# Kernel tuning notes

Measured on AMD Instinct MI355X. Metric: run time of the kernel, lower is better.

Reference implementation:

```python
import jax, jax.numpy as jnp
from jax import lax
import numpy as np

B, N, DIM = 2, 2048, 1024
HEADS, DIM_HEAD = 16, 64
KERNELS = (0, 3, 5, 7)
GROUPS = len(KERNELS)
HPG = HEADS // GROUPS          # heads per group = 4
CG = HPG * DIM_HEAD            # channels per group for depthwise conv = 256
INNER = HEADS * DIM_HEAD       # 1024


def _alibi_slopes(n):
    # power-of-2 branch of LearnedAlibiPosBias._get_slopes (n=4 here)
    start = 2.0 ** (-(2.0 ** -(np.log2(n) - 3)))
    return np.array([start * start ** i for i in range(n)], dtype=np.float32)


def setup_inputs() -> dict:
    key = jax.random.key(0)
    ks = jax.random.split(key, 24)
    d = {}
    d['x'] = jax.random.normal(ks[0], (B, N, DIM), jnp.float32)
    d['ln_gamma'] = jnp.ones((DIM,), jnp.float32)
    d['ln_beta'] = jnp.zeros((DIM,), jnp.float32)
    d['w_qkv'] = jax.random.normal(ks[1], (3 * INNER, DIM), jnp.float32) * 0.02
    i = 2
    for p in ('q', 'k', 'v'):
        for ksz in (3, 5, 7):
            d[f'dw{p}_w{ksz}'] = jax.random.normal(ks[i], (CG, 1, ksz), jnp.float32) * 0.1; i += 1
            d[f'dw{p}_b{ksz}'] = jax.random.normal(ks[i], (CG,), jnp.float32) * 0.02; i += 1
    # learned alibi slopes, initialized to the standard ALiBi values per group
    sl = _alibi_slopes(HPG).reshape(1, HPG, 1, 1)
    d['slopes'] = jnp.asarray(np.tile(sl, (GROUPS, 1, 1, 1)))
    d['w_out'] = jax.random.normal(ks[20], (DIM, INNER), jnp.float32) * 0.02
    return d


def _dw_causal_conv(xg, w, b, ksz):
    # xg: (B, CG, N); depthwise causal conv, left pad ksz-1
    xg = jnp.pad(xg, ((0, 0), (0, 0), (ksz - 1, 0)))
    out = lax.conv_general_dilated(xg, w, (1,), 'VALID',
                                   feature_group_count=CG,
                                   dimension_numbers=('NCH', 'OIH', 'NCH'))
    return out + b[None, :, None]


def _grouped_conv(t, w3, b3, w5, b5, w7, b7):
    # t: (B, INNER, N) channels laid out head-major; group g = channels [g*CG,(g+1)*CG)
    parts = [t[:, :CG]]  # group 0: kernel_size 0 -> Identity
    for i, (w, b, ksz) in enumerate(((w3, b3, 3), (w5, b5, 5), (w7, b7, 7))):
        parts.append(_dw_causal_conv(t[:, (i + 1) * CG:(i + 2) * CG], w, b, ksz))
    out = jnp.concatenate(parts, axis=1)                      # (B, INNER, N)
    out = out.reshape(B, HEADS, DIM_HEAD, N)
    return jnp.transpose(out, (0, 1, 3, 2))                   # (B, H, N, Dh)


def _forward(x, ln_gamma, ln_beta, w_qkv,
             dwq_w3, dwq_b3, dwq_w5, dwq_b5, dwq_w7, dwq_b7,
             dwk_w3, dwk_b3, dwk_w5, dwk_b5, dwk_w7, dwk_b7,
             dwv_w3, dwv_b3, dwv_w5, dwv_b5, dwv_w7, dwv_b7,
             slopes, w_out):
    scale = DIM_HEAD ** -0.5
    mu = jnp.mean(x, axis=-1, keepdims=True)
    var = jnp.var(x, axis=-1, keepdims=True)
    h = (x - mu) * lax.rsqrt(var + 1e-5) * ln_gamma + ln_beta   # (B, N, DIM)
    qkv = jnp.einsum('bnd,ed->ben', h, w_qkv)                   # (B, 3*INNER, N)
    q, k, v = jnp.split(qkv, 3, axis=1)
    q = _grouped_conv(q, dwq_w3, dwq_b3, dwq_w5, dwq_b5, dwq_w7, dwq_b7)
    k = _grouped_conv(k, dwk_w3, dwk_b3, dwk_w5, dwk_b5, dwk_w7, dwk_b7)
    v = _grouped_conv(v, dwv_w3, dwv_b3, dwv_w5, dwv_b5, dwv_w7, dwv_b7)
    sim = jnp.einsum('bhid,bhjd->bhij', q * scale, k)           # (B, H, N, N)
    idx = jnp.arange(N)
    dist = -jnp.abs(idx[None, :] - idx[:, None]).astype(sim.dtype)  # (N, N)
    bias = slopes.reshape(HEADS, 1, 1) * dist[None]             # (H, N, N)
    sim = sim + bias[None]
    causal = idx[None, :] > idx[:, None]                        # strictly future
    sim = jnp.where(causal[None, None], -jnp.finfo(sim.dtype).max, sim)
    attn = jax.nn.softmax(sim, axis=-1)
    out = jnp.einsum('bhij,bhjd->bhid', attn, v)                # (B, H, N, Dh)
    out = jnp.transpose(out, (0, 2, 1, 3)).reshape(B, N, INNER)
    return jnp.einsum('bne,de->bnd', out, w_out)


def reference(x, ln_gamma, ln_beta, w_qkv,
              dwq_w3, dwq_b3, dwq_w5, dwq_b5, dwq_w7, dwq_b7,
              dwk_w3, dwk_b3, dwk_w5, dwk_b5, dwk_w7, dwk_b7,
              dwv_w3, dwv_b3, dwv_w5, dwv_b5, dwv_w7, dwv_b7,
              slopes, w_out):
    return _forward(x, ln_gamma, ln_beta, w_qkv,
                    dwq_w3, dwq_b3, dwq_w5, dwq_b5, dwq_w7, dwq_b7,
                    dwk_w3, dwk_b3, dwk_w5, dwk_b5, dwk_w7, dwk_b7,
                    dwv_w3, dwv_b3, dwv_w5, dwv_b5, dwv_w7, dwv_b7,
                    slopes, w_out)
```

## Files before the change

### kernel.cpp

```cpp
#include <hip/hip_runtime.h>
#include <hip/hip_bf16.h>
#include <stdint.h>

typedef __bf16 bf8 __attribute__((ext_vector_type(8)));
typedef float  f4  __attribute__((ext_vector_type(4)));

constexpr int BATCH  = 2;
constexpr int SEQ    = 2048;
constexpr int DMODEL = 1024;
constexpr int NH     = 16;
constexpr int DHEAD  = 64;
constexpr int E3     = 3072;

static __device__ __forceinline__ f4 mfma16(bf8 a, bf8 b, f4 c){
  return __builtin_amdgcn_mfma_f32_16x16x32_bf16(a, b, c, 0, 0, 0);
}
static __device__ __forceinline__ uint32_t pack2(float a, float b){
  union { __bf16 h[2]; uint32_t u; } p;
  p.h[0] = (__bf16)a; p.h[1] = (__bf16)b;
  return p.u;
}
typedef const __attribute__((address_space(1))) uint32_t g_u32;
typedef __attribute__((address_space(3))) uint32_t l_u32;
static __device__ __forceinline__ void glds16(const __bf16* g, __bf16* l){
  __builtin_amdgcn_global_load_lds((g_u32*)g, (l_u32*)l, 16, 0, 0);
}

__global__ __launch_bounds__(256) void cvt_kernel(const float* __restrict__ s,
                                                  __bf16* __restrict__ d, int n){
  int i = (blockIdx.x * 256 + threadIdx.x) * 4;
  if(i < n){
    float4 v = *(const float4*)(s + i);
    __bf16 o[4] = {(__bf16)v.x, (__bf16)v.y, (__bf16)v.z, (__bf16)v.w};
    *(uint2*)(d + i) = *(const uint2*)o;
  }
}

__global__ __launch_bounds__(256) void ln_kernel(const float* __restrict__ x,
                                                 const float* __restrict__ gam,
                                                 const float* __restrict__ bet,
                                                 __bf16* __restrict__ h){
  int row = blockIdx.x;
  int tid = threadIdx.x;
  const float* xr = x + (size_t)row * DMODEL;
  float4 v = *(const float4*)(xr + tid*4);
  float s = v.x + v.y + v.z + v.w;
  float ss = v.x*v.x + v.y*v.y + v.z*v.z + v.w*v.w;
#pragma unroll
  for(int m=1;m<64;m<<=1){ s += __shfl_xor(s, m); ss += __shfl_xor(ss, m); }
  __shared__ float sm[8];
  int wid = tid >> 6;
  if((tid & 63) == 0){ sm[wid] = s; sm[4+wid] = ss; }
  __syncthreads();
  s  = sm[0]+sm[1]+sm[2]+sm[3];
  ss = sm[4]+sm[5]+sm[6]+sm[7];
  float mu  = s * (1.f/DMODEL);
  float var = ss * (1.f/DMODEL) - mu*mu;
  float r = rsqrtf(var + 1e-5f);
  float4 g = *(const float4*)(gam + tid*4);
  float4 bb = *(const float4*)(bet + tid*4);
  __bf16 o[4] = { (__bf16)((v.x-mu)*r*g.x + bb.x), (__bf16)((v.y-mu)*r*g.y + bb.y),
                  (__bf16)((v.z-mu)*r*g.z + bb.z), (__bf16)((v.w-mu)*r*g.w + bb.w) };
  *(uint2*)(h + (size_t)row*DMODEL + tid*4) = *(uint2*)o;
}

template<typename CT>
__global__ __launch_bounds__(256) void gemm_nt(const __bf16* __restrict__ A,
                                               const __bf16* __restrict__ Bm,
                                               CT* __restrict__ C,
                                               int M, int Ncols, int K){
  __shared__ __align__(16) __bf16 As[128*32];
  __shared__ __align__(16) __bf16 Bs[128*32];
  int m0 = blockIdx.y * 128, n0 = blockIdx.x * 128;
  int tid = threadIdx.x;
  int lane = tid & 63, wid = tid >> 6;
  int quad = lane >> 4, l15 = lane & 15;
  int wm = (wid >> 1) * 64, wn = (wid & 1) * 64;
  f4 acc[4][4] = {};
  int r0 = wid*32 + (lane >> 2);
  int cofs = (lane & 3) * 8;
  const __bf16* ag = A  + (size_t)(m0 + r0) * K + cofs;
  const __bf16* bg = Bm + (size_t)(n0 + r0) * K + cofs;
  __bf16* asb0 = &As[(wid*32)*32];
  __bf16* asb1 = &As[(wid*32+16)*32];
  __bf16* bsb0 = &Bs[(wid*32)*32];
  __bf16* bsb1 = &Bs[(wid*32+16)*32];
  const size_t rowskip = (size_t)16 * K;
  for(int k0 = 0; k0 < K; k0 += 32){
    __syncthreads();
    glds16(ag + k0,           asb0);
    glds16(ag + rowskip + k0, asb1);
    glds16(bg + k0,           bsb0);
    glds16(bg + rowskip + k0, bsb1);
    __syncthreads();
    bf8 af[4], bfr[4];
#pragma unroll
    for(int i=0;i<4;i++){
      af[i]  = *(const bf8*)&As[(wm + i*16 + l15)*32 + quad*8];
      bfr[i] = *(const bf8*)&Bs[(wn + i*16 + l15)*32 + quad*8];
    }
#pragma unroll
    for(int mi=0;mi<4;mi++)
#pragma unroll
      for(int ni=0;ni<4;ni++)
        acc[mi][ni] = mfma16(af[mi], bfr[ni], acc[mi][ni]);
  }
#pragma unroll
  for(int mi=0;mi<4;mi++)
#pragma unroll
    for(int ni=0;ni<4;ni++)
#pragma unroll
      for(int r=0;r<4;r++){
        int row = m0 + wm + mi*16 + quad*4 + r;
        int col = n0 + wn + ni*16 + l15;
        C[(size_t)row*Ncols + col] = (CT)acc[mi][ni][r];
      }
}

template<typename CT>
__global__ __launch_bounds__(256) void gemm_nt64(const __bf16* __restrict__ A,
                                                 const __bf16* __restrict__ Bm,
                                                 CT* __restrict__ C,
                                                 int M, int Ncols, int K){
  __shared__ __align__(16) __bf16 As[128*32];
  __shared__ __align__(16) __bf16 Bs[64*32];
  int m0 = blockIdx.y * 128, n0 = blockIdx.x * 64;
  int tid = threadIdx.x;
  int lane = tid & 63, wid = tid >> 6;
  int quad = lane >> 4, l15 = lane & 15;
  int wm = wid * 32;
  f4 acc[2][4] = {};
  int ra = wid*32 + (lane >> 2);
  int rb = wid*16 + (lane >> 2);
  int cofs = (lane & 3) * 8;
  const __bf16* ag = A  + (size_t)(m0 + ra) * K + cofs;
  const __bf16* bg = Bm + (size_t)(n0 + rb) * K + cofs;
  __bf16* asb0 = &As[(wid*32)*32];
  __bf16* asb1 = &As[(wid*32+16)*32];
  __bf16* bsb  = &Bs[(wid*16)*32];
  const size_t rowskip = (size_t)16 * K;
  for(int k0 = 0; k0 < K; k0 += 32){
    __syncthreads();
    glds16(ag + k0,           asb0);
    glds16(ag + rowskip + k0, asb1);
    glds16(bg + k0,           bsb);
    __syncthreads();
    bf8 af[2], bfr[4];
#pragma unroll
    for(int i=0;i<2;i++)
      af[i]  = *(const bf8*)&As[(wm + i*16 + l15)*32 + quad*8];
#pragma unroll
    for(int i=0;i<4;i++)
      bfr[i] = *(const bf8*)&Bs[(i*16 + l15)*32 + quad*8];
#pragma unroll
    for(int mi=0;mi<2;mi++)
#pragma unroll
      for(int ni=0;ni<4;ni++)
        acc[mi][ni] = mfma16(af[mi], bfr[ni], acc[mi][ni]);
  }
#pragma unroll
  for(int mi=0;mi<2;mi++)
#pragma unroll
    for(int ni=0;ni<4;ni++)
#pragma unroll
      for(int r=0;r<4;r++){
        int row = m0 + wm + mi*16 + quad*4 + r;
        int col = n0 + ni*16 + l15;
        C[(size_t)row*Ncols + col] = (CT)acc[mi][ni][r];
      }
}

__global__ __launch_bounds__(256) void conv_kernel(const __bf16* __restrict__ qkv,
    __bf16* __restrict__ qo, __bf16* __restrict__ ko, __bf16* __restrict__ vt,
    const float* qw3,const float* qb3,const float* qw5,const float* qb5,const float* qw7,const float* qb7,
    const float* kw3,const float* kb3,const float* kw5,const float* kb5,const float* kw7,const float* kb7,
    const float* vw3,const float* vb3,const float* vw5,const float* vb5,const float* vw7,const float* vb7){
  __shared__ __align__(16) __bf16 tile[72*256];
  int nc = blockIdx.x;
  int ec = blockIdx.y;
  int b  = blockIdx.z;
  int tid = threadIdx.x;
  int n0 = nc * 64;
  {
    int rrow = tid >> 5;
    int ccol = (tid & 31) * 8;
    const __bf16* src = qkv + (size_t)b*SEQ*E3 + ec*256 + ccol;
#pragma unroll
    for(int p=0;p<9;p++){
      int row = p*8 + rrow;
      int n = n0 - 8 + row;
      uint4 v = {0u,0u,0u,0u};
      if(n >= 0) v = *(const uint4*)(src + (size_t)n*E3);
      *(uint4*)&tile[row*256 + ccol] = v;
    }
  }
  __syncthreads();
  int e = ec*256 + tid;
  int p  = e >> 10;
  int c  = e & 1023;
  int g  = c >> 8;
  int cg = c & 255;
  int hh = c >> 6;
  int dh = c & 63;
  const float* W[9]  = {qw3,qw5,qw7,kw3,kw5,kw7,vw3,vw5,vw7};
  const float* Bp[9] = {qb3,qb5,qb7,kb3,kb5,kb7,vb3,vb5,vb7};
  int ksz = (g==0)?0:((g==1)?3:((g==2)?5:7));
  float w[7] = {0,0,0,0,0,0,0};
  float bias = 0.f;
  if(g > 0){
    const float* wp = W[p*3 + g - 1];
    const float* bp = Bp[p*3 + g - 1];
    for(int t=0;t<ksz;t++) w[t] = wp[cg*ksz + t];
    bias = bp[cg];
  }
  float xh[6];
#pragma unroll
  for(int i=0;i<6;i++) xh[i] = (float)tile[(2+i)*256 + tid];
  if(p == 2){
    __bf16* ob = vt + ((size_t)((b*NH + hh)*DHEAD + dh))*SEQ + n0;
    for(int blk=0; blk<8; blk++){
      __bf16 tmp[8];
#pragma unroll
      for(int u=0;u<8;u++){
        int dn = blk*8 + u;
        float cur = (float)tile[(8+dn)*256 + tid];
        float o;
        if(ksz == 0)      o = cur;
        else if(ksz == 3) o = w[0]*xh[4] + w[1]*xh[5] + w[2]*cur + bias;
        else if(ksz == 5) o = w[0]*xh[2] + w[1]*xh[3] + w[2]*xh[4] + w[3]*xh[5] + w[4]*cur + bias;
        else              o = w[0]*xh[0] + w[1]*xh[1] + w[2]*xh[2] + w[3]*xh[3] + w[4]*xh[4] + w[5]*xh[5] + w[6]*cur + bias;
        xh[0]=xh[1]; xh[1]=xh[2]; xh[2]=xh[3]; xh[3]=xh[4]; xh[4]=xh[5]; xh[5]=cur;
        tmp[u] = (__bf16)o;
      }
      *(uint4*)(ob + blk*8) = *(const uint4*)tmp;
    }
  } else {
    __bf16* outp = (p==0) ? qo : ko;
    __bf16* op = outp + ((size_t)(b*NH + hh)*SEQ)*DHEAD + dh;
#pragma unroll 4
    for(int dn=0; dn<64; dn++){
      float cur = (float)tile[(8+dn)*256 + tid];
      float o;
      if(ksz == 0)      o = cur;
      else if(ksz == 3) o = w[0]*xh[4] + w[1]*xh[5] + w[2]*cur + bias;
      else if(ksz == 5) o = w[0]*xh[2] + w[1]*xh[3] + w[2]*xh[4] + w[3]*xh[5] + w[4]*cur + bias;
      else              o = w[0]*xh[0] + w[1]*xh[1] + w[2]*xh[2] + w[3]*xh[3] + w[4]*xh[4] + w[5]*xh[5] + w[6]*cur + bias;
      xh[0]=xh[1]; xh[1]=xh[2]; xh[2]=xh[3]; xh[3]=xh[4]; xh[4]=xh[5]; xh[5]=cur;
      op[(size_t)(n0+dn)*DHEAD] = (__bf16)o;
    }
  }
}

__global__ __launch_bounds__(256) void attn_kernel(const __bf16* __restrict__ Qin,
                                                   const __bf16* __restrict__ Kin,
                                                   const __bf16* __restrict__ Vtin,
                                                   const float* __restrict__ slopes,
                                                   __bf16* __restrict__ Oout){
  __shared__ __align__(16) __bf16 Ks[2][64*72];
  __shared__ __align__(16) __bf16 Vts[2][64*72];
  __shared__ __align__(16) __bf16 Ps[4][16*72];
  __shared__ float Al[4][16];
  int bid = blockIdx.x;
  int pr = bid >> 5;
  int by = (bid & 7) + ((bid >> 3) & 3) * 8;
  int b  = by >> 4, hh = by & 15;
  int tid = threadIdx.x, lane = tid & 63, w = tid >> 6;
  int quad = lane >> 4, l15 = lane & 15;
  const __bf16* qb  = Qin  + (size_t)by * SEQ * DHEAD;
  const __bf16* kb  = Kin  + (size_t)by * SEQ * DHEAD;
  const __bf16* vtb = Vtin + (size_t)by * DHEAD * SEQ;
  const float L2E = 1.4426950408889634f;
  float slope = slopes[hh];
  const float c1 = 0.125f * L2E;
  float c2 = slope * L2E;
  float cjb[16];
#pragma unroll
  for(int jt=0;jt<4;jt++)
#pragma unroll
    for(int r=0;r<4;r++)
      cjb[jt*4+r] = c2 * (float)(jt*16 + quad*4 + r);

  int r1 = tid >> 3;
  int co = (tid & 7) * 8;
  const __bf16* kg0 = kb  + (size_t)r1*DHEAD + co;
  const __bf16* vg0 = vtb + (size_t)r1*SEQ  + co;
  int ko1 = r1*72 + co, ko2 = (r1+32)*72 + co;

  for(int ph=0; ph<2; ph++){
    int qi = ph ? (31 - pr) : pr;
    int q0 = qi * 64;
    int nst = qi + 1;
    int i0 = q0 + w*16;
    int i  = i0 + l15;
    bf8 aq0 = *(const bf8*)(qb + (size_t)(i0 + l15)*DHEAD + quad*8);
    bf8 aq1 = *(const bf8*)(qb + (size_t)(i0 + l15)*DHEAD + 32 + quad*8);
    f4 oacc[4] = {};
    float l_ = 0.f;
    {
      uint4 ka  = *(const uint4*)(kg0);
      uint4 kb2 = *(const uint4*)(kg0 + (size_t)32*DHEAD);
      uint4 va  = *(const uint4*)(vg0);
      uint4 vb2 = *(const uint4*)(vg0 + (size_t)32*SEQ);
      *(uint4*)&Ks[0][ko1]  = ka;  *(uint4*)&Ks[0][ko2]  = kb2;
      *(uint4*)&Vts[0][ko1] = va;  *(uint4*)&Vts[0][ko2] = vb2;
    }
    __syncthreads();
    const __bf16* kgt = kg0 + (size_t)64*DHEAD;
    const __bf16* vgt = vg0 + 64;
    int cur = 0;
    for(int t=0; t<nst; t++){
      int j0 = t*64;
      uint4 ka, kb2, va, vb2;
      bool pf = (t+1) < nst;
      if(pf){
        ka  = *(const uint4*)(kgt);
        kb2 = *(const uint4*)(kgt + (size_t)32*DHEAD);
        va  = *(const uint4*)(vgt);
        vb2 = *(const uint4*)(vgt + (size_t)32*SEQ);
        kgt += (size_t)64*DHEAD; vgt += 64;
      }
      const __bf16* KsC  = Ks[cur];
      const __bf16* VtsC = Vts[cur];
      f4 s[4] = {};
#pragma unroll
      for(int jt=0;jt<4;jt++){
        bf8 ak0 = *(const bf8*)&KsC[(jt*16+l15)*72 + quad*8];
        bf8 ak1 = *(const bf8*)&KsC[(jt*16+l15)*72 + 32 + quad*8];
        s[jt] = mfma16(ak0, aq0, s[jt]);
        s[jt] = mfma16(ak1, aq1, s[jt]);
      }
      float sv[4][4];
      if(t < nst-1){
        float cdi = c2 * (float)(i - j0) + 8.0f;
#pragma unroll
        for(int jt=0;jt<4;jt++)
#pragma unroll
          for(int r=0;r<4;r++)
            sv[jt][r] = fmaf(s[jt][r], c1, cjb[jt*4+r] - cdi);
      } else {
#pragma unroll
        for(int jt=0;jt<4;jt++)
#pragma unroll
          for(int r=0;r<4;r++){
            int j = j0 + jt*16 + quad*4 + r;
            int d = i - j;
            float val = fmaf(s[jt][r], c1, -fmaf(c2, (float)d, 8.0f));
            sv[jt][r] = (d < 0) ? -1e30f : val;
          }
      }
      float lsum = 0.f;
#pragma unroll
      for(int jt=0;jt<4;jt++){
        float p0 = __builtin_amdgcn_exp2f(sv[jt][0]);
        float p1 = __builtin_amdgcn_exp2f(sv[jt][1]);
        float p2 = __builtin_amdgcn_exp2f(sv[jt][2]);
        float p3 = __builtin_amdgcn_exp2f(sv[jt][3]);
        lsum += (p0+p1)+(p2+p3);
        uint2 pk = { pack2(p0,p1), pack2(p2,p3) };
        *(uint2*)&Ps[w][l15*72 + jt*16 + quad*4] = pk;
      }
      lsum += __shfl_xor(lsum, 16);
      lsum += __shfl_xor(lsum, 32);
      l_ += lsum;
#pragma unroll
      for(int jk=0;jk<2;jk++){
        bf8 ap = *(const bf8*)&Ps[w][l15*72 + jk*32 + quad*8];
#pragma unroll
        for(int nd=0;nd<4;nd++){
          bf8 bv = *(const bf8*)&VtsC[(nd*16+l15)*72 + jk*32 + quad*8];
          oacc[nd] = mfma16(ap, bv, oacc[nd]);
        }
      }
      if(pf){
        int nb = cur ^ 1;
        *(uint4*)&Ks[nb][ko1]  = ka;  *(uint4*)&Ks[nb][ko2]  = kb2;
        *(uint4*)&Vts[nb][ko1] = va;  *(uint4*)&Vts[nb][ko2] = vb2;
      }
      __syncthreads();
      cur ^= 1;
    }
    if(quad == 0) Al[w][l15] = 1.0f / l_;
    f4 linv = *(const f4*)&Al[w][quad*4];
#pragma unroll
    for(int nd=0;nd<4;nd++)
#pragma unroll
      for(int r=0;r<4;r++){
        int io = i0 + quad*4 + r;
        Oout[((size_t)(b*SEQ + io))*DMODEL + hh*64 + nd*16 + l15] =
            (__bf16)(oacc[nd][r] * linv[r]);
      }
  }
}

extern "C" void kernel_launch(void* const* d_in, const int* in_sizes, int n_in,
                              void* d_out, int out_size, void* d_ws, size_t ws_size,
                              hipStream_t stream){
  const float* x      = (const float*)d_in[0];
  const float* gam    = (const float*)d_in[1];
  const float* bet    = (const float*)d_in[2];
  const float* w_qkv  = (const float*)d_in[3];
  const float* slopes = (const float*)d_in[22];
  const float* w_out  = (const float*)d_in[23];
  float* out = (float*)d_out;

  char* ws = (char*)d_ws;
  __bf16* h       = (__bf16*)(ws);
  __bf16* qpost   = (__bf16*)(ws);
  __bf16* qkv     = (__bf16*)(ws + ((size_t)8  << 20));
  __bf16* att     = (__bf16*)(ws + ((size_t)8  << 20));
  __bf16* wout_bf = (__bf16*)(ws + ((size_t)24 << 20));
  __bf16* wqkv_bf = (__bf16*)(ws + ((size_t)32 << 20));
  __bf16* kpost   = (__bf16*)(ws + ((size_t)32 << 20));
  __bf16* vtp     = (__bf16*)(ws + ((size_t)40 << 20));

  constexpr int NQKV = 3 * DMODEL * DMODEL;
  constexpr int NOUT = DMODEL * DMODEL;

  cvt_kernel<<<NQKV/4/256, 256, 0, stream>>>(w_qkv, wqkv_bf, NQKV);
  ln_kernel<<<BATCH*SEQ, 256, 0, stream>>>(x, gam, bet, h);
  gemm_nt<__bf16><<<dim3(E3/128, (BATCH*SEQ)/128), 256, 0, stream>>>(
      h, wqkv_bf, qkv, BATCH*SEQ, E3, DMODEL);
  conv_kernel<<<dim3(32, 12, BATCH), 256, 0, stream>>>(qkv, qpost, kpost, vtp,
    (const float*)d_in[4],(const float*)d_in[5],(const float*)d_in[6],(const float*)d_in[7],
    (const float*)d_in[8],(const float*)d_in[9],
    (const float*)d_in[10],(const float*)d_in[11],(const float*)d_in[12],(const float*)d_in[13],
    (const float*)d_in[14],(const float*)d_in[15],
    (const float*)d_in[16],(const float*)d_in[17],(const float*)d_in[18],(const float*)d_in[19],
    (const float*)d_in[20],(const float*)d_in[21]);
  cvt_kernel<<<NOUT/4/256, 256, 0, stream>>>(w_out, wout_bf, NOUT);
  attn_kernel<<<dim3(512), 256, 0, stream>>>(qpost, kpost, vtp, slopes, att);
  gemm_nt64<float><<<dim3(DMODEL/64, (BATCH*SEQ)/128), 256, 0, stream>>>(
      att, wout_bf, out, BATCH*SEQ, DMODEL, DMODEL);
}
```

Measured before the change: 248.0 us.

## Shrink attention blocks to 2 waves, swizzle K/V LDS, add MFMA priority hints

The attention kernel moves from 256-thread blocks handling 64 query rows to 128-thread blocks handling 32 rows, launching 1024 blocks instead of 512. Causal tile pairing now runs over 32-row query tiles. The padded 72-stride K/V shared-memory layout becomes a 64-stride XOR-swizzled layout, which aims to avoid bank conflicts while cutting LDS use. s_setprio is raised around the MFMA sections. This adds occupancy and finer load balance, but each block now loads whole 64-key tiles to serve only 32 queries, which doubles K/V traffic per query.

```diff
diff --git a/kernel.cpp b/kernel.cpp
--- a/kernel.cpp
+++ b/kernel.cpp
@@ -251,18 +251,18 @@
   }
 }
 
-__global__ __launch_bounds__(256) void attn_kernel(const __bf16* __restrict__ Qin,
+__global__ __launch_bounds__(128) void attn_kernel(const __bf16* __restrict__ Qin,
                                                    const __bf16* __restrict__ Kin,
                                                    const __bf16* __restrict__ Vtin,
                                                    const float* __restrict__ slopes,
                                                    __bf16* __restrict__ Oout){
-  __shared__ __align__(16) __bf16 Ks[2][64*72];
-  __shared__ __align__(16) __bf16 Vts[2][64*72];
-  __shared__ __align__(16) __bf16 Ps[4][16*72];
-  __shared__ float Al[4][16];
+  __shared__ __align__(16) __bf16 Ks[2][64*64];
+  __shared__ __align__(16) __bf16 Vts[2][64*64];
+  __shared__ __align__(16) __bf16 Ps[2][16*72];
+  __shared__ float Al[2][16];
   int bid = blockIdx.x;
-  int pr = bid >> 5;
-  int by = (bid & 7) + ((bid >> 3) & 3) * 8;
+  int slot = bid >> 5;
+  int by   = bid & 31;
   int b  = by >> 4, hh = by & 15;
   int tid = threadIdx.x, lane = tid & 63, w = tid >> 6;
   int quad = lane >> 4, l15 = lane & 15;
@@ -280,29 +280,42 @@
     for(int r=0;r<4;r++)
       cjb[jt*4+r] = c2 * (float)(jt*16 + quad*4 + r);
 
+  int sxq0 = ((quad     ^ (l15 & 7)) << 3);
+  int sxq1 = (((quad+4) ^ (l15 & 7)) << 3);
+
   int r1 = tid >> 3;
-  int co = (tid & 7) * 8;
-  const __bf16* kg0 = kb  + (size_t)r1*DHEAD + co;
-  const __bf16* vg0 = vtb + (size_t)r1*SEQ  + co;
-  int ko1 = r1*72 + co, ko2 = (r1+32)*72 + co;
+  int c8 = tid & 7;
+  int swz = ((c8 ^ (r1 & 7)) << 3);
+  const __bf16* kg0 = kb  + (size_t)r1*DHEAD + c8*8;
+  const __bf16* vg0 = vtb + (size_t)r1*SEQ  + c8*8;
+  int lo0 = (r1     )*64 + swz;
+  int lo1 = (r1 + 16)*64 + swz;
+  int lo2 = (r1 + 32)*64 + swz;
+  int lo3 = (r1 + 48)*64 + swz;
 
   for(int ph=0; ph<2; ph++){
-    int qi = ph ? (31 - pr) : pr;
-    int q0 = qi * 64;
-    int nst = qi + 1;
+    int qt = ph ? (63 - slot) : slot;
+    int q0 = qt * 32;
+    int nst = (qt >> 1) + 1;
     int i0 = q0 + w*16;
     int i  = i0 + l15;
-    bf8 aq0 = *(const bf8*)(qb + (size_t)(i0 + l15)*DHEAD + quad*8);
-    bf8 aq1 = *(const bf8*)(qb + (size_t)(i0 + l15)*DHEAD + 32 + quad*8);
+    bf8 aq0 = *(const bf8*)(qb + (size_t)i*DHEAD + quad*8);
+    bf8 aq1 = *(const bf8*)(qb + (size_t)i*DHEAD + 32 + quad*8);
     f4 oacc[4] = {};
     float l_ = 0.f;
     {
-      uint4 ka  = *(const uint4*)(kg0);
-      uint4 kb2 = *(const uint4*)(kg0 + (size_t)32*DHEAD);
-      uint4 va  = *(const uint4*)(vg0);
-      uint4 vb2 = *(const uint4*)(vg0 + (size_t)32*SEQ);
-      *(uint4*)&Ks[0][ko1]  = ka;  *(uint4*)&Ks[0][ko2]  = kb2;
-      *(uint4*)&Vts[0][ko1] = va;  *(uint4*)&Vts[0][ko2] = vb2;
+      uint4 k0v = *(const uint4*)(kg0);
+      uint4 k1v = *(const uint4*)(kg0 + (size_t)16*DHEAD);
+      uint4 k2v = *(const uint4*)(kg0 + (size_t)32*DHEAD);
+      uint4 k3v = *(const uint4*)(kg0 + (size_t)48*DHEAD);
+      uint4 v0v = *(const uint4*)(vg0);
+      uint4 v1v = *(const uint4*)(vg0 + (size_t)16*SEQ);
+      uint4 v2v = *(const uint4*)(vg0 + (size_t)32*SEQ);
+      uint4 v3v = *(const uint4*)(vg0 + (size_t)48*SEQ);
+      *(uint4*)&Ks[0][lo0]  = k0v; *(uint4*)&Ks[0][lo1]  = k1v;
+      *(uint4*)&Ks[0][lo2]  = k2v; *(uint4*)&Ks[0][lo3]  = k3v;
+      *(uint4*)&Vts[0][lo0] = v0v; *(uint4*)&Vts[0][lo1] = v1v;
+      *(uint4*)&Vts[0][lo2] = v2v; *(uint4*)&Vts[0][lo3] = v3v;
     }
     __syncthreads();
     const __bf16* kgt = kg0 + (size_t)64*DHEAD;
@@ -310,25 +323,31 @@
     int cur = 0;
     for(int t=0; t<nst; t++){
       int j0 = t*64;
-      uint4 ka, kb2, va, vb2;
+      uint4 k0v, k1v, k2v, k3v, v0v, v1v, v2v, v3v;
       bool pf = (t+1) < nst;
       if(pf){
-        ka  = *(const uint4*)(kgt);
-        kb2 = *(const uint4*)(kgt + (size_t)32*DHEAD);
-        va  = *(const uint4*)(vgt);
-        vb2 = *(const uint4*)(vgt + (size_t)32*SEQ);
+        k0v = *(const uint4*)(kgt);
+        k1v = *(const uint4*)(kgt + (size_t)16*DHEAD);
+        k2v = *(const uint4*)(kgt + (size_t)32*DHEAD);
+        k3v = *(const uint4*)(kgt + (size_t)48*DHEAD);
+        v0v = *(const uint4*)(vgt);
+        v1v = *(const uint4*)(vgt + (size_t)16*SEQ);
+        v2v = *(const uint4*)(vgt + (size_t)32*SEQ);
+        v3v = *(const uint4*)(vgt + (size_t)48*SEQ);
         kgt += (size_t)64*DHEAD; vgt += 64;
       }
       const __bf16* KsC  = Ks[cur];
       const __bf16* VtsC = Vts[cur];
       f4 s[4] = {};
+      __builtin_amdgcn_s_setprio(1);
 #pragma unroll
       for(int jt=0;jt<4;jt++){
-        bf8 ak0 = *(const bf8*)&KsC[(jt*16+l15)*72 + quad*8];
-        bf8 ak1 = *(const bf8*)&KsC[(jt*16+l15)*72 + 32 + quad*8];
+        bf8 ak0 = *(const bf8*)&KsC[(jt*16+l15)*64 + sxq0];
+        bf8 ak1 = *(const bf8*)&KsC[(jt*16+l15)*64 + sxq1];
         s[jt] = mfma16(ak0, aq0, s[jt]);
         s[jt] = mfma16(ak1, aq1, s[jt]);
       }
+      __builtin_amdgcn_s_setprio(0);
       float sv[4][4];
       if(t < nst-1){
         float cdi = c2 * (float)(i - j0) + 8.0f;
@@ -362,19 +381,23 @@
       lsum += __shfl_xor(lsum, 16);
       lsum += __shfl_xor(lsum, 32);
       l_ += lsum;
+      __builtin_amdgcn_s_setprio(1);
 #pragma unroll
       for(int jk=0;jk<2;jk++){
         bf8 ap = *(const bf8*)&Ps[w][l15*72 + jk*32 + quad*8];
 #pragma unroll
         for(int nd=0;nd<4;nd++){
-          bf8 bv = *(const bf8*)&VtsC[(nd*16+l15)*72 + jk*32 + quad*8];
+          bf8 bv = *(const bf8*)&VtsC[(nd*16+l15)*64 + (((jk*4+quad) ^ (l15&7))<<3)];
           oacc[nd] = mfma16(ap, bv, oacc[nd]);
         }
       }
+      __builtin_amdgcn_s_setprio(0);
       if(pf){
         int nb = cur ^ 1;
-        *(uint4*)&Ks[nb][ko1]  = ka;  *(uint4*)&Ks[nb][ko2]  = kb2;
-        *(uint4*)&Vts[nb][ko1] = va;  *(uint4*)&Vts[nb][ko2] = vb2;
+        *(uint4*)&Ks[nb][lo0]  = k0v; *(uint4*)&Ks[nb][lo1]  = k1v;
+        *(uint4*)&Ks[nb][lo2]  = k2v; *(uint4*)&Ks[nb][lo3]  = k3v;
+        *(uint4*)&Vts[nb][lo0] = v0v; *(uint4*)&Vts[nb][lo1] = v1v;
+        *(uint4*)&Vts[nb][lo2] = v2v; *(uint4*)&Vts[nb][lo3] = v3v;
       }
       __syncthreads();
       cur ^= 1;
@@ -428,7 +451,7 @@
     (const float*)d_in[16],(const float*)d_in[17],(const float*)d_in[18],(const float*)d_in[19],
     (const float*)d_in[20],(const float*)d_in[21]);
   cvt_kernel<<<NOUT/4/256, 256, 0, stream>>>(w_out, wout_bf, NOUT);
-  attn_kernel<<<dim3(512), 256, 0, stream>>>(qpost, kpost, vtp, slopes, att);
+  attn_kernel<<<dim3(1024), 128, 0, stream>>>(qpost, kpost, vtp, slopes, att);
   gemm_nt64<float><<<dim3(DMODEL/64, (BATCH*SEQ)/128), 256, 0, stream>>>(
       att, wout_bf, out, BATCH*SEQ, DMODEL, DMODEL);
 }
```

New measurement: 252.4 us. Within noise of the previous version (+1.8%).

## Use 128-wide KV tiles with direct global-to-LDS loads and swizzled LDS

Applied to the files above, without the earlier changes.

The attention kernel now processes 128 keys per iteration instead of 64, which halves the number of loop iterations and barriers. K and V tiles are loaded straight into LDS with glds16 async loads into XOR-swizzled, unpadded layouts, in place of register-staged uint4 copies. The softmax/PV stage is split into two 64-key halves, with s_setprio raised around the MFMA sections, and launch bounds now ask for 2 blocks per CU. In exchange, LDS use grows, the causal tile can waste up to half its work, and register pressure rises with s[8] and the preloaded V fragments.

```diff
diff --git a/kernel.cpp b/kernel.cpp
--- a/kernel.cpp
+++ b/kernel.cpp
@@ -251,13 +251,13 @@
   }
 }
 
-__global__ __launch_bounds__(256) void attn_kernel(const __bf16* __restrict__ Qin,
-                                                   const __bf16* __restrict__ Kin,
-                                                   const __bf16* __restrict__ Vtin,
-                                                   const float* __restrict__ slopes,
-                                                   __bf16* __restrict__ Oout){
-  __shared__ __align__(16) __bf16 Ks[2][64*72];
-  __shared__ __align__(16) __bf16 Vts[2][64*72];
+__global__ __launch_bounds__(256, 2) void attn_kernel(const __bf16* __restrict__ Qin,
+                                                      const __bf16* __restrict__ Kin,
+                                                      const __bf16* __restrict__ Vtin,
+                                                      const float* __restrict__ slopes,
+                                                      __bf16* __restrict__ Oout){
+  __shared__ __align__(16) __bf16 Ks[2][128*64];
+  __shared__ __align__(16) __bf16 Vts[2][64*128];
   __shared__ __align__(16) __bf16 Ps[4][16*72];
   __shared__ float Al[4][16];
   int bid = blockIdx.x;
@@ -273,6 +273,7 @@
   float slope = slopes[hh];
   const float c1 = 0.125f * L2E;
   float c2 = slope * L2E;
+  float c2_64 = c2 * 64.f;
   float cjb[16];
 #pragma unroll
   for(int jt=0;jt<4;jt++)
@@ -280,102 +281,118 @@
     for(int r=0;r<4;r++)
       cjb[jt*4+r] = c2 * (float)(jt*16 + quad*4 + r);
 
-  int r1 = tid >> 3;
-  int co = (tid & 7) * 8;
-  const __bf16* kg0 = kb  + (size_t)r1*DHEAD + co;
-  const __bf16* vg0 = vtb + (size_t)r1*SEQ  + co;
-  int ko1 = r1*72 + co, ko2 = (r1+32)*72 + co;
+  int sxq0 = ((quad     ^ (l15 & 7)) << 3);
+  int sxq1 = (((quad+4) ^ (l15 & 7)) << 3);
+
+  const __bf16* ksrc = kb + (size_t)(lane>>3)*DHEAD + ((lane&7) ^ ((lane>>3)&7))*8;
+  const __bf16* vsrc[4];
+#pragma unroll
+  for(int u=0;u<4;u++){
+    int g = w*4 + u;
+    int vrow = g*4 + (lane>>4);
+    vsrc[u] = vtb + (size_t)vrow*SEQ + (((lane&15) ^ (vrow&15)) * 8);
+  }
 
   for(int ph=0; ph<2; ph++){
     int qi = ph ? (31 - pr) : pr;
     int q0 = qi * 64;
-    int nst = qi + 1;
+    int nst = (qi >> 1) + 1;
     int i0 = q0 + w*16;
     int i  = i0 + l15;
-    bf8 aq0 = *(const bf8*)(qb + (size_t)(i0 + l15)*DHEAD + quad*8);
-    bf8 aq1 = *(const bf8*)(qb + (size_t)(i0 + l15)*DHEAD + 32 + quad*8);
+    bf8 aq0 = *(const bf8*)(qb + (size_t)i*DHEAD + quad*8);
+    bf8 aq1 = *(const bf8*)(qb + (size_t)i*DHEAD + 32 + quad*8);
     f4 oacc[4] = {};
     float l_ = 0.f;
-    {
-      uint4 ka  = *(const uint4*)(kg0);
-      uint4 kb2 = *(const uint4*)(kg0 + (size_t)32*DHEAD);
-      uint4 va  = *(const uint4*)(vg0);
-      uint4 vb2 = *(const uint4*)(vg0 + (size_t)32*SEQ);
-      *(uint4*)&Ks[0][ko1]  = ka;  *(uint4*)&Ks[0][ko2]  = kb2;
-      *(uint4*)&Vts[0][ko1] = va;  *(uint4*)&Vts[0][ko2] = vb2;
+#pragma unroll
+    for(int u=0;u<4;u++){
+      int g = w*4 + u;
+      glds16(ksrc + (size_t)g*8*DHEAD, &Ks[0][g*512]);
+      glds16(vsrc[u],                  &Vts[0][g*512]);
     }
     __syncthreads();
-    const __bf16* kgt = kg0 + (size_t)64*DHEAD;
-    const __bf16* vgt = vg0 + 64;
     int cur = 0;
     for(int t=0; t<nst; t++){
-      int j0 = t*64;
-      uint4 ka, kb2, va, vb2;
+      int j0 = t*128;
       bool pf = (t+1) < nst;
       if(pf){
-        ka  = *(const uint4*)(kgt);
-        kb2 = *(const uint4*)(kgt + (size_t)32*DHEAD);
-        va  = *(const uint4*)(vgt);
-        vb2 = *(const uint4*)(vgt + (size_t)32*SEQ);
-        kgt += (size_t)64*DHEAD; vgt += 64;
+        int nb = cur ^ 1;
+#pragma unroll
+        for(int u=0;u<4;u++){
+          int g = w*4 + u;
+          glds16(ksrc + (size_t)((t+1)*128 + g*8)*DHEAD, &Ks[nb][g*512]);
+          glds16(vsrc[u] + (t+1)*128,                    &Vts[nb][g*512]);
+        }
       }
       const __bf16* KsC  = Ks[cur];
       const __bf16* VtsC = Vts[cur];
-      f4 s[4] = {};
-#pragma unroll
-      for(int jt=0;jt<4;jt++){
-        bf8 ak0 = *(const bf8*)&KsC[(jt*16+l15)*72 + quad*8];
-        bf8 ak1 = *(const bf8*)&KsC[(jt*16+l15)*72 + 32 + quad*8];
+      f4 s[8] = {};
+      __builtin_amdgcn_s_setprio(1);
+#pragma unroll
+      for(int jt=0;jt<8;jt++){
+        bf8 ak0 = *(const bf8*)&KsC[(jt*16+l15)*64 + sxq0];
+        bf8 ak1 = *(const bf8*)&KsC[(jt*16+l15)*64 + sxq1];
         s[jt] = mfma16(ak0, aq0, s[jt]);
         s[jt] = mfma16(ak1, aq1, s[jt]);
       }
-      float sv[4][4];
-      if(t < nst-1){
-        float cdi = c2 * (float)(i - j0) + 8.0f;
-#pragma unroll
-        for(int jt=0;jt<4;jt++)
-#pragma unroll
-          for(int r=0;r<4;r++)
-            sv[jt][r] = fmaf(s[jt][r], c1, cjb[jt*4+r] - cdi);
-      } else {
-#pragma unroll
-        for(int jt=0;jt<4;jt++)
-#pragma unroll
-          for(int r=0;r<4;r++){
-            int j = j0 + jt*16 + quad*4 + r;
-            int d = i - j;
-            float val = fmaf(s[jt][r], c1, -fmaf(c2, (float)d, 8.0f));
-            sv[jt][r] = (d < 0) ? -1e30f : val;
+      __builtin_amdgcn_s_setprio(0);
+      float lsum = 0.f;
+      bool masked = (t == nst-1);
+      float cdi = c2 * (float)(i - j0) + 8.0f;
+#pragma unroll
+      for(int h=0;h<2;h++){
+        bf8 bv[2][4];
+#pragma unroll
+        for(int jj=0;jj<2;jj++){
+          int jk = h*2 + jj;
+#pragma unroll
+          for(int nd=0;nd<4;nd++)
+            bv[jj][nd] = *(const bf8*)&VtsC[(nd*16+l15)*128 + (((jk*4+quad) ^ l15) << 3)];
+        }
+        float sv[4][4];
+        if(!masked){
+#pragma unroll
+          for(int jl=0;jl<4;jl++){
+            int jt = h*4 + jl;
+#pragma unroll
+            for(int r=0;r<4;r++)
+              sv[jl][r] = fmaf(s[jt][r], c1, cjb[jl*4+r] - cdi + (h ? c2_64 : 0.f));
           }
-      }
-      float lsum = 0.f;
-#pragma unroll
-      for(int jt=0;jt<4;jt++){
-        float p0 = __builtin_amdgcn_exp2f(sv[jt][0]);
-        float p1 = __builtin_amdgcn_exp2f(sv[jt][1]);
-        float p2 = __builtin_amdgcn_exp2f(sv[jt][2]);
-        float p3 = __builtin_amdgcn_exp2f(sv[jt][3]);
-        lsum += (p0+p1)+(p2+p3);
-        uint2 pk = { pack2(p0,p1), pack2(p2,p3) };
-        *(uint2*)&Ps[w][l15*72 + jt*16 + quad*4] = pk;
+        } else {
+#pragma unroll
+          for(int jl=0;jl<4;jl++){
+            int jt = h*4 + jl;
+#pragma unroll
+            for(int r=0;r<4;r++){
+              int j = j0 + jt*16 + quad*4 + r;
+              int d = i - j;
+              float val = fmaf(s[jt][r], c1, -fmaf(c2, (float)d, 8.0f));
+              sv[jl][r] = (d < 0) ? -1e30f : val;
+            }
+          }
+        }
+#pragma unroll
+        for(int jl=0;jl<4;jl++){
+          float p0 = __builtin_amdgcn_exp2f(sv[jl][0]);
+          float p1 = __builtin_amdgcn_exp2f(sv[jl][1]);
+          float p2 = __builtin_amdgcn_exp2f(sv[jl][2]);
+          float p3 = __builtin_amdgcn_exp2f(sv[jl][3]);
+          lsum += (p0+p1)+(p2+p3);
+          uint2 pk = { pack2(p0,p1), pack2(p2,p3) };
+          *(uint2*)&Ps[w][l15*72 + jl*16 + quad*4] = pk;
+        }
+        __builtin_amdgcn_s_setprio(1);
+#pragma unroll
+        for(int jj=0;jj<2;jj++){
+          bf8 ap = *(const bf8*)&Ps[w][l15*72 + jj*32 + quad*8];
+#pragma unroll
+          for(int nd=0;nd<4;nd++)
+            oacc[nd] = mfma16(ap, bv[jj][nd], oacc[nd]);
+        }
+        __builtin_amdgcn_s_setprio(0);
       }
       lsum += __shfl_xor(lsum, 16);
       lsum += __shfl_xor(lsum, 32);
       l_ += lsum;
-#pragma unroll
-      for(int jk=0;jk<2;jk++){
-        bf8 ap = *(const bf8*)&Ps[w][l15*72 + jk*32 + quad*8];
-#pragma unroll
-        for(int nd=0;nd<4;nd++){
-          bf8 bv = *(const bf8*)&VtsC[(nd*16+l15)*72 + jk*32 + quad*8];
-          oacc[nd] = mfma16(ap, bv, oacc[nd]);
-        }
-      }
-      if(pf){
-        int nb = cur ^ 1;
-        *(uint4*)&Ks[nb][ko1]  = ka;  *(uint4*)&Ks[nb][ko2]  = kb2;
-        *(uint4*)&Vts[nb][ko1] = va;  *(uint4*)&Vts[nb][ko2] = vb2;
-      }
       __syncthreads();
       cur ^= 1;
     }
@@ -389,6 +406,7 @@
         Oout[((size_t)(b*SEQ + io))*DMODEL + hh*64 + nd*16 + l15] =
             (__bf16)(oacc[nd][r] * linv[r]);
       }
+    if(ph == 0) __syncthreads();
   }
 }
 
```

Measured after the change: 252.0 us. Within noise of the previous version (+1.6%).
